# Optimization experiments

Measured on AMD Instinct MI355X. Metric: run time of the kernel, lower is better.

The kernel has to match this reference:

```python
import jax, jax.numpy as jnp
import numpy as np

NUM_EXPERTS = 8
TOP_K = 2
ENTROPY_WEIGHT = 0.1
MAX_USAGE_RATIO = 0.3


def setup_inputs() -> dict:
    key = jax.random.key(0)
    k0, k1, k2 = jax.random.split(key, 3)
    B, S, D, H, E = 4, 4096, 1024, 1024, NUM_EXPERTS
    x = jax.random.normal(k0, (B, S, D), jnp.float32)
    gate_w = jax.random.normal(k1, (D, E), jnp.float32) * (1.0 / np.sqrt(D))
    gate_b = jnp.zeros((E,), jnp.float32)
    expert_w = jax.random.normal(k2, (E, D, H), jnp.float32) * (1.0 / np.sqrt(D))
    expert_b = jnp.zeros((E, H), jnp.float32)
    return {"x": x, "gate_w": gate_w, "gate_b": gate_b,
            "expert_w": expert_w, "expert_b": expert_b}


def reference(x, gate_w, gate_b, expert_w, expert_b):
    # x: [B, S, D]; dropout omitted (eval mode / deterministic reference)
    B, S, D = x.shape
    E = gate_w.shape[1]
    H = expert_w.shape[2]
    N = B * S
    xf = x.reshape(N, D)

    gate_logits = xf @ gate_w + gate_b            # [N, E]
    gate_probs = jax.nn.softmax(gate_logits, axis=-1)
    entropy = -jnp.sum(gate_probs * jnp.log(gate_probs + 1e-10), axis=-1).mean()
    entropy_loss = ENTROPY_WEIGHT * entropy

    topk_probs, topk_idx = jax.lax.top_k(gate_probs, TOP_K)   # [N, K]
    onehot = jax.nn.one_hot(topk_idx, E, dtype=xf.dtype)       # [N, K, E]
    combine = jnp.einsum('nk,nke->ne', topk_probs, onehot)     # [N, E] gating weight per expert

    # Weighted combine of per-expert Linear outputs; loop over small fixed E.
    out = jnp.zeros((N, H), xf.dtype)
    for e in range(E):
        out = out + combine[:, e:e + 1] * (xf @ expert_w[e] + expert_b[e])

    counts = jnp.sum(onehot, axis=(0, 1))                      # [E] tokens routed per expert
    usage_ratios = counts / N
    overuse_penalty = jnp.sum(jax.nn.relu(usage_ratios - MAX_USAGE_RATIO))

    return out.reshape(B, S, H), entropy_loss + overuse_penalty
```

## Files before the change

### kernel.cpp

```cpp
#include <hip/hip_runtime.h>
#include <hip/hip_bf16.h>

typedef __bf16 bf16x8 __attribute__((ext_vector_type(8)));
typedef __bf16 bf16x4 __attribute__((ext_vector_type(4)));
typedef float  f32x4  __attribute__((ext_vector_type(4)));

#define NTOK 16384
#define DDIM 1024
#define HDIM 1024
#define NEXP 8

#define XB_OFF   0u
#define WT_OFF   33554432u
#define IDX_OFF  50331648u
#define PRB_OFF  50855936u
#define TTE_OFF  51380224u
#define TTP_OFF  51511296u
#define CNT_OFF  51642368u
#define ENT_OFF  51642400u

typedef __attribute__((address_space(1))) void gvoid_t;
typedef __attribute__((address_space(3))) void lvoid_t;

__device__ __forceinline__ void cp16(void* lds, const void* g) {
  __builtin_amdgcn_global_load_lds((gvoid_t*)g, (lvoid_t*)lds, 16, 0, 0);
}

__global__ __launch_bounds__(256) void transpose_w(const float* __restrict__ w,
                                                   __bf16* __restrict__ wT) {
  const int e  = blockIdx.z;
  const int d0 = blockIdx.y * 64;
  const int h0 = blockIdx.x * 64;
  __shared__ float tile[64][68];
  const int t = threadIdx.x;
  const float* base = w + ((size_t)e * DDIM + d0) * HDIM + h0;
#pragma unroll
  for (int it = 0; it < 4; ++it) {
    int dl = it * 16 + (t >> 4);
    int hl = (t & 15) * 4;
    float4 v = *(const float4*)(base + (size_t)dl * HDIM + hl);
    tile[dl][hl]     = v.x;
    tile[dl][hl + 1] = v.y;
    tile[dl][hl + 2] = v.z;
    tile[dl][hl + 3] = v.w;
  }
  __syncthreads();
  __bf16* obase = wT + ((size_t)e * HDIM + h0) * DDIM + d0;
#pragma unroll
  for (int it = 0; it < 4; ++it) {
    int hl = it * 16 + (t >> 4);
    int dl = (t & 15) * 4;
    bf16x4 bv;
    bv[0] = (__bf16)tile[dl][hl];
    bv[1] = (__bf16)tile[dl + 1][hl];
    bv[2] = (__bf16)tile[dl + 2][hl];
    bv[3] = (__bf16)tile[dl + 3][hl];
    *(bf16x4*)(obase + (size_t)hl * DDIM + dl) = bv;
  }
}

__global__ __launch_bounds__(256) void gate_kernel(
    const float* __restrict__ x, const float* __restrict__ gw,
    const float* __restrict__ gb, __bf16* __restrict__ xb,
    int* __restrict__ idx_g, float* __restrict__ prob_g,
    int2* __restrict__ tt_e, float2* __restrict__ tt_p,
    int* __restrict__ cnt_g, float* __restrict__ ent_g) {
  __shared__ float gwT[8 * 1040];
  __shared__ int   lidx[8 * 64];
  __shared__ float lprob[8 * 64];
  __shared__ int   lcnt[8];
  __shared__ int   gbase[8];
  __shared__ float went[4];
  const int tid = threadIdx.x, w = tid >> 6, lane = tid & 63;
  if (tid < 8) lcnt[tid] = 0;
#pragma unroll
  for (int i = 0; i < 32; ++i) {
    int lin = i * 256 + tid;
    gwT[(lin & 7) * 1040 + (lin >> 3)] = gw[lin];
  }
  __syncthreads();

  float entacc = 0.f;
  for (int t = 0; t < 8; ++t) {
    const int n = blockIdx.x * 32 + w * 8 + t;
    const float4* xr = (const float4*)(x + (size_t)n * DDIM);
    float acc[8] = {0.f, 0.f, 0.f, 0.f, 0.f, 0.f, 0.f, 0.f};
#pragma unroll
    for (int i = 0; i < 4; ++i) {
      float4 v = xr[i * 64 + lane];
      bf16x4 bv;
      bv[0] = (__bf16)v.x; bv[1] = (__bf16)v.y;
      bv[2] = (__bf16)v.z; bv[3] = (__bf16)v.w;
      *(bf16x4*)(xb + (size_t)n * DDIM + i * 256 + lane * 4) = bv;
#pragma unroll
      for (int e = 0; e < 8; ++e) {
        float4 g = *(const float4*)&gwT[e * 1040 + i * 256 + lane * 4];
        acc[e] += v.x * g.x + v.y * g.y + v.z * g.z + v.w * g.w;
      }
    }
#pragma unroll
    for (int e = 0; e < 8; ++e) {
      float s = acc[e];
      for (int off = 32; off; off >>= 1) s += __shfl_down(s, off);
      acc[e] = s;
    }
    if (lane == 0) {
      float p[8];
      float mx = -1e30f;
#pragma unroll
      for (int e = 0; e < 8; ++e) { p[e] = acc[e] + gb[e]; mx = fmaxf(mx, p[e]); }
      float s = 0.f;
#pragma unroll
      for (int e = 0; e < 8; ++e) { p[e] = expf(p[e] - mx); s += p[e]; }
      float inv = 1.0f / s;
      float ent = 0.f;
#pragma unroll
      for (int e = 0; e < 8; ++e) { p[e] *= inv; ent -= p[e] * logf(p[e] + 1e-10f); }
      entacc += ent;
      int e1 = 0; float p1 = p[0];
#pragma unroll
      for (int e = 1; e < 8; ++e) if (p[e] > p1) { p1 = p[e]; e1 = e; }
      int e2 = (e1 == 0) ? 1 : 0; float p2 = p[e2];
#pragma unroll
      for (int e = 0; e < 8; ++e) if (e != e1 && p[e] > p2) { p2 = p[e]; e2 = e; }
      tt_e[n] = make_int2(e1, e2);
      tt_p[n] = make_float2(p1, p2);
      int j = atomicAdd(&lcnt[e1], 1); lidx[e1 * 64 + j] = n; lprob[e1 * 64 + j] = p1;
      j = atomicAdd(&lcnt[e2], 1);     lidx[e2 * 64 + j] = n; lprob[e2 * 64 + j] = p2;
    }
  }
  if (lane == 0) went[w] = entacc;
  __syncthreads();
  if (tid < 8) gbase[tid] = atomicAdd(&cnt_g[tid], lcnt[tid]);
  if (tid == 0) atomicAdd(ent_g, went[0] + went[1] + went[2] + went[3]);
  __syncthreads();
#pragma unroll
  for (int e = 0; e < 8; ++e) {
    for (int j = tid; j < lcnt[e]; j += 256) {
      idx_g[e * NTOK + gbase[e] + j]  = lidx[e * 64 + j];
      prob_g[e * NTOK + gbase[e] + j] = lprob[e * 64 + j];
    }
  }
}

__global__ __launch_bounds__(256) void init_out(const int2* __restrict__ tt_e,
                                                const float2* __restrict__ tt_p,
                                                const float* __restrict__ eb,
                                                float* __restrict__ out) {
  const int n = blockIdx.x, t = threadIdx.x;
  int2   ee = tt_e[n];
  float2 pp = tt_p[n];
  float4 v1 = ((const float4*)(eb + (size_t)ee.x * HDIM))[t];
  float4 v2 = ((const float4*)(eb + (size_t)ee.y * HDIM))[t];
  float4 r;
  r.x = pp.x * v1.x + pp.y * v2.x;
  r.y = pp.x * v1.y + pp.y * v2.y;
  r.z = pp.x * v1.z + pp.y * v2.z;
  r.w = pp.x * v1.w + pp.y * v2.w;
  ((float4*)(out + (size_t)n * HDIM))[t] = r;
}

__global__ __launch_bounds__(256) void moe_gemm(
    const __bf16* __restrict__ xb, const __bf16* __restrict__ wT,
    const int* __restrict__ idx_g, const float* __restrict__ prob_g,
    const int* __restrict__ cnt_g, float* __restrict__ out) {
  const int e = blockIdx.z, gy = blockIdx.y, gx = blockIdx.x;
  const int cnt = cnt_g[e];
  if (gy * 128 >= cnt) return;

  __shared__ __bf16 Ash[128 * 64];
  __shared__ __bf16 Bsh[128 * 64];
  __shared__ int    tok_s[128];
  __shared__ float  p_s[128];

  const int tid = threadIdx.x, w = tid >> 6, lane = tid & 63;
  if (tid < 128) {
    int gm  = gy * 128 + tid;
    int src = (gm < cnt) ? gm : (cnt - 1);
    tok_s[tid] = idx_g[e * NTOK + src];
    p_s[tid]   = (gm < cnt) ? prob_g[e * NTOK + src] : 0.0f;
  }
  __syncthreads();

  f32x4 acc[4][4];
  const f32x4 zero = {0.f, 0.f, 0.f, 0.f};
#pragma unroll
  for (int mi = 0; mi < 4; ++mi)
#pragma unroll
    for (int ni = 0; ni < 4; ++ni) acc[mi][ni] = zero;

  const __bf16* wbase = wT + (size_t)e * HDIM * DDIM + (size_t)(gx * 128) * DDIM;
  const int wm = (w >> 1) * 64, wn = (w & 1) * 64;
  const int tq = lane >> 4, tr = lane & 15;
  const int rsub = lane >> 3, c = lane & 7;

  for (int kk = 0; kk < 16; ++kk) {
    const int k0 = kk * 64;
#pragma unroll
    for (int it = 0; it < 4; ++it) {
      int rb = it * 32 + w * 8;
      int r  = rb + rsub;
      cp16((char*)Ash + rb * 128,
           xb + (size_t)tok_s[r] * DDIM + k0 + c * 8);
    }
#pragma unroll
    for (int it = 0; it < 4; ++it) {
      int rb = it * 32 + w * 8;
      int r  = rb + rsub;
      cp16((char*)Bsh + rb * 128,
           wbase + (size_t)r * DDIM + k0 + c * 8);
    }
    __syncthreads();
#pragma unroll
    for (int h = 0; h < 2; ++h) {
      bf16x8 a[4], b[4];
#pragma unroll
      for (int mi = 0; mi < 4; ++mi)
        a[mi] = *(const bf16x8*)((const char*)Ash + (wm + mi * 16 + tr) * 128 + h * 64 + tq * 16);
#pragma unroll
      for (int ni = 0; ni < 4; ++ni)
        b[ni] = *(const bf16x8*)((const char*)Bsh + (wn + ni * 16 + tr) * 128 + h * 64 + tq * 16);
#pragma unroll
      for (int mi = 0; mi < 4; ++mi)
#pragma unroll
        for (int ni = 0; ni < 4; ++ni)
          acc[mi][ni] = __builtin_amdgcn_mfma_f32_16x16x32_bf16(a[mi], b[ni], acc[mi][ni], 0, 0, 0);
    }
    __syncthreads();
  }

#pragma unroll
  for (int mi = 0; mi < 4; ++mi) {
#pragma unroll
    for (int r = 0; r < 4; ++r) {
      int lr = wm + mi * 16 + tq * 4 + r;
      int gm = gy * 128 + lr;
      if (gm < cnt) {
        int   tok = tok_s[lr];
        float p   = p_s[lr];
        float* orow = out + (size_t)tok * HDIM + gx * 128 + wn + tr;
#pragma unroll
        for (int ni = 0; ni < 4; ++ni)
          atomicAdd(orow + ni * 16, p * acc[mi][ni][r]);
      }
    }
  }
}

__global__ void finalize(const float* __restrict__ ent_g, const int* __restrict__ cnt_g,
                         float* __restrict__ loss_out) {
  if (threadIdx.x == 0) {
    float ent = ent_g[0] / (float)NTOK;
    float pen = 0.f;
    for (int e = 0; e < 8; ++e) {
      float r = (float)cnt_g[e] / (float)NTOK - 0.3f;
      if (r > 0.f) pen += r;
    }
    loss_out[0] = 0.1f * ent + pen;
  }
}

extern "C" void kernel_launch(void* const* d_in, const int* in_sizes, int n_in,
                              void* d_out, int out_size, void* d_ws, size_t ws_size,
                              hipStream_t stream) {
  const float* x  = (const float*)d_in[0];
  const float* gw = (const float*)d_in[1];
  const float* gb = (const float*)d_in[2];
  const float* ew = (const float*)d_in[3];
  const float* eb = (const float*)d_in[4];
  float* out = (float*)d_out;
  char*  ws  = (char*)d_ws;

  __bf16* xb     = (__bf16*)(ws + XB_OFF);
  __bf16* wT     = (__bf16*)(ws + WT_OFF);
  int*    idx_g  = (int*)(ws + IDX_OFF);
  float*  prob_g = (float*)(ws + PRB_OFF);
  int2*   tt_e   = (int2*)(ws + TTE_OFF);
  float2* tt_p   = (float2*)(ws + TTP_OFF);
  int*    cnt_g  = (int*)(ws + CNT_OFF);
  float*  ent_g  = (float*)(ws + ENT_OFF);

  hipMemsetAsync(ws + CNT_OFF, 0, 64, stream);
  transpose_w<<<dim3(16, 16, 8), 256, 0, stream>>>(ew, wT);
  gate_kernel<<<dim3(NTOK / 32), 256, 0, stream>>>(x, gw, gb, xb, idx_g, prob_g,
                                                   tt_e, tt_p, cnt_g, ent_g);
  init_out<<<dim3(NTOK), 256, 0, stream>>>(tt_e, tt_p, eb, out);
  moe_gemm<<<dim3(8, 128, 8), 256, 0, stream>>>(xb, wT, idx_g, prob_g, cnt_g, out);
  finalize<<<1, 64, 0, stream>>>(ent_g, cnt_g, out + (size_t)NTOK * HDIM);
}
```

Measured before the change: 344.1 us.

## Group tokens by expert pair so each GEMM tile computes both experts and stores directly

Tokens are now bucketed by their (expert_lo, expert_hi) pair instead of per expert. A scan kernel builds a tile list and a scatter kernel builds the token permutation. Each GEMM block loads one A tile and two weight tiles, accumulates both experts, adds the biases and writes the output with plain stores. This removes the init_out pass and the float atomics on the output. LDS is XOR-swizzled to avoid bank conflicts, and the gate kernel keeps its weights in registers. The costs are a doubled accumulator footprint (register pressure, lower occupancy), two extra small launches, and possible tail waste because the 64 pair buckets each pad up to 128 rows.

```diff
diff --git a/kernel.cpp b/kernel.cpp
--- a/kernel.cpp
+++ b/kernel.cpp
@@ -8,16 +8,21 @@
 #define NTOK 16384
 #define DDIM 1024
 #define HDIM 1024
-#define NEXP 8
+#define CNT_STRIDE 16
 
 #define XB_OFF   0u
 #define WT_OFF   33554432u
-#define IDX_OFF  50331648u
-#define PRB_OFF  50855936u
-#define TTE_OFF  51380224u
-#define TTP_OFF  51511296u
-#define CNT_OFF  51642368u
-#define ENT_OFF  51642400u
+#define IDXP_OFF 50331648u
+#define PPP_OFF  50397184u
+#define TPID_OFF 50528256u
+#define TPP_OFF  50593792u
+#define CNT_OFF  50724864u
+#define CUR_OFF  50728960u
+#define BASE_OFF 50733056u
+#define TILT_OFF 50733312u
+#define NT_OFF   50736384u
+#define ENT_OFF  50736388u
+#define ZERO_LEN 11536u
 
 typedef __attribute__((address_space(1))) void gvoid_t;
 typedef __attribute__((address_space(3))) void lvoid_t;
@@ -28,9 +33,10 @@
 
 __global__ __launch_bounds__(256) void transpose_w(const float* __restrict__ w,
                                                    __bf16* __restrict__ wT) {
-  const int e  = blockIdx.z;
-  const int d0 = blockIdx.y * 64;
-  const int h0 = blockIdx.x * 64;
+  const int b  = blockIdx.x;
+  const int e  = b >> 8;
+  const int d0 = ((b >> 4) & 15) * 64;
+  const int h0 = (b & 15) * 64;
   __shared__ float tile[64][68];
   const int t = threadIdx.x;
   const float* base = w + ((size_t)e * DDIM + d0) * HDIM + h0;
@@ -62,202 +68,243 @@
 __global__ __launch_bounds__(256) void gate_kernel(
     const float* __restrict__ x, const float* __restrict__ gw,
     const float* __restrict__ gb, __bf16* __restrict__ xb,
-    int* __restrict__ idx_g, float* __restrict__ prob_g,
-    int2* __restrict__ tt_e, float2* __restrict__ tt_p,
+    int* __restrict__ tt_pid, float2* __restrict__ tt_pp,
     int* __restrict__ cnt_g, float* __restrict__ ent_g) {
-  __shared__ float gwT[8 * 1040];
-  __shared__ int   lidx[8 * 64];
-  __shared__ float lprob[8 * 64];
-  __shared__ int   lcnt[8];
-  __shared__ int   gbase[8];
+  __shared__ float gwT[8 * 1024];
+  __shared__ int   lcnt[64];
   __shared__ float went[4];
   const int tid = threadIdx.x, w = tid >> 6, lane = tid & 63;
-  if (tid < 8) lcnt[tid] = 0;
+  for (int i = tid; i < 64; i += 256) lcnt[i] = 0;
 #pragma unroll
   for (int i = 0; i < 32; ++i) {
     int lin = i * 256 + tid;
-    gwT[(lin & 7) * 1040 + (lin >> 3)] = gw[lin];
-  }
-  __syncthreads();
+    gwT[(lin & 7) * 1024 + (lin >> 3)] = gw[lin];
+  }
+  __syncthreads();
+  float4 gr[4][8];
+#pragma unroll
+  for (int j = 0; j < 4; ++j)
+#pragma unroll
+    for (int e = 0; e < 8; ++e)
+      gr[j][e] = *(const float4*)&gwT[e * 1024 + j * 256 + lane * 4];
+  float gbr[8];
+#pragma unroll
+  for (int e = 0; e < 8; ++e) gbr[e] = gb[e];
 
   float entacc = 0.f;
-  for (int t = 0; t < 8; ++t) {
-    const int n = blockIdx.x * 32 + w * 8 + t;
-    const float4* xr = (const float4*)(x + (size_t)n * DDIM);
+  for (int t = 0; t < 4; ++t) {
+    const int n = blockIdx.x * 16 + w * 4 + t;
     float acc[8] = {0.f, 0.f, 0.f, 0.f, 0.f, 0.f, 0.f, 0.f};
 #pragma unroll
-    for (int i = 0; i < 4; ++i) {
-      float4 v = xr[i * 64 + lane];
+    for (int j = 0; j < 4; ++j) {
+      float4 v = *(const float4*)(x + (size_t)n * DDIM + j * 256 + lane * 4);
       bf16x4 bv;
       bv[0] = (__bf16)v.x; bv[1] = (__bf16)v.y;
       bv[2] = (__bf16)v.z; bv[3] = (__bf16)v.w;
-      *(bf16x4*)(xb + (size_t)n * DDIM + i * 256 + lane * 4) = bv;
+      *(bf16x4*)(xb + (size_t)n * DDIM + j * 256 + lane * 4) = bv;
 #pragma unroll
       for (int e = 0; e < 8; ++e) {
-        float4 g = *(const float4*)&gwT[e * 1040 + i * 256 + lane * 4];
+        float4 g = gr[j][e];
         acc[e] += v.x * g.x + v.y * g.y + v.z * g.z + v.w * g.w;
       }
     }
 #pragma unroll
     for (int e = 0; e < 8; ++e) {
       float s = acc[e];
-      for (int off = 32; off; off >>= 1) s += __shfl_down(s, off);
+#pragma unroll
+      for (int off = 1; off < 64; off <<= 1) s += __shfl_xor(s, off);
       acc[e] = s;
     }
+    float p[8];
+    float mx = -1e30f;
+#pragma unroll
+    for (int e = 0; e < 8; ++e) { p[e] = acc[e] + gbr[e]; mx = fmaxf(mx, p[e]); }
+    float s = 0.f;
+#pragma unroll
+    for (int e = 0; e < 8; ++e) { p[e] = expf(p[e] - mx); s += p[e]; }
+    float inv = 1.0f / s;
+    float ent = 0.f;
+#pragma unroll
+    for (int e = 0; e < 8; ++e) { p[e] *= inv; ent -= p[e] * logf(p[e] + 1e-10f); }
+    entacc += ent;
+    int e1 = 0; float p1 = p[0];
+#pragma unroll
+    for (int e = 1; e < 8; ++e) if (p[e] > p1) { p1 = p[e]; e1 = e; }
+    int e2 = (e1 == 0) ? 1 : 0; float p2 = p[e2];
+#pragma unroll
+    for (int e = 0; e < 8; ++e) if (e != e1 && p[e] > p2) { p2 = p[e]; e2 = e; }
+    int   elo = (e1 < e2) ? e1 : e2;
+    int   ehi = (e1 < e2) ? e2 : e1;
+    float plo = (e1 < e2) ? p1 : p2;
+    float phi = (e1 < e2) ? p2 : p1;
+    int pid = elo * 8 + ehi;
     if (lane == 0) {
-      float p[8];
-      float mx = -1e30f;
-#pragma unroll
-      for (int e = 0; e < 8; ++e) { p[e] = acc[e] + gb[e]; mx = fmaxf(mx, p[e]); }
-      float s = 0.f;
-#pragma unroll
-      for (int e = 0; e < 8; ++e) { p[e] = expf(p[e] - mx); s += p[e]; }
-      float inv = 1.0f / s;
-      float ent = 0.f;
-#pragma unroll
-      for (int e = 0; e < 8; ++e) { p[e] *= inv; ent -= p[e] * logf(p[e] + 1e-10f); }
-      entacc += ent;
-      int e1 = 0; float p1 = p[0];
-#pragma unroll
-      for (int e = 1; e < 8; ++e) if (p[e] > p1) { p1 = p[e]; e1 = e; }
-      int e2 = (e1 == 0) ? 1 : 0; float p2 = p[e2];
-#pragma unroll
-      for (int e = 0; e < 8; ++e) if (e != e1 && p[e] > p2) { p2 = p[e]; e2 = e; }
-      tt_e[n] = make_int2(e1, e2);
-      tt_p[n] = make_float2(p1, p2);
-      int j = atomicAdd(&lcnt[e1], 1); lidx[e1 * 64 + j] = n; lprob[e1 * 64 + j] = p1;
-      j = atomicAdd(&lcnt[e2], 1);     lidx[e2 * 64 + j] = n; lprob[e2 * 64 + j] = p2;
+      tt_pid[n] = pid;
+      tt_pp[n]  = make_float2(plo, phi);
+      atomicAdd(&lcnt[pid], 1);
     }
   }
   if (lane == 0) went[w] = entacc;
   __syncthreads();
-  if (tid < 8) gbase[tid] = atomicAdd(&cnt_g[tid], lcnt[tid]);
-  if (tid == 0) atomicAdd(ent_g, went[0] + went[1] + went[2] + went[3]);
-  __syncthreads();
-#pragma unroll
-  for (int e = 0; e < 8; ++e) {
-    for (int j = tid; j < lcnt[e]; j += 256) {
-      idx_g[e * NTOK + gbase[e] + j]  = lidx[e * 64 + j];
-      prob_g[e * NTOK + gbase[e] + j] = lprob[e * 64 + j];
-    }
-  }
-}
-
-__global__ __launch_bounds__(256) void init_out(const int2* __restrict__ tt_e,
-                                                const float2* __restrict__ tt_p,
-                                                const float* __restrict__ eb,
-                                                float* __restrict__ out) {
-  const int n = blockIdx.x, t = threadIdx.x;
-  int2   ee = tt_e[n];
-  float2 pp = tt_p[n];
-  float4 v1 = ((const float4*)(eb + (size_t)ee.x * HDIM))[t];
-  float4 v2 = ((const float4*)(eb + (size_t)ee.y * HDIM))[t];
-  float4 r;
-  r.x = pp.x * v1.x + pp.y * v2.x;
-  r.y = pp.x * v1.y + pp.y * v2.y;
-  r.z = pp.x * v1.z + pp.y * v2.z;
-  r.w = pp.x * v1.w + pp.y * v2.w;
-  ((float4*)(out + (size_t)n * HDIM))[t] = r;
+  if (tid < 64 && lcnt[tid]) atomicAdd(&cnt_g[tid * CNT_STRIDE], lcnt[tid]);
+  if (tid == 0)
+    atomicAdd(ent_g, went[0] + went[1] + went[2] + went[3]);
+}
+
+__global__ void scan_kernel(const int* __restrict__ cnt_g, int* __restrict__ base_g,
+                            int4* __restrict__ tilt, int* __restrict__ nt_g,
+                            const float* __restrict__ ent_g, float* __restrict__ loss_out) {
+  if (threadIdx.x == 0) {
+    int b = 0, t = 0;
+    int ecnt[8] = {0, 0, 0, 0, 0, 0, 0, 0};
+    for (int pid = 0; pid < 64; ++pid) {
+      int c = cnt_g[pid * CNT_STRIDE];
+      base_g[pid] = b;
+      if (c > 0) {
+        ecnt[pid >> 3] += c;
+        ecnt[pid & 7]  += c;
+        for (int r = 0; r < c; r += 128) tilt[t++] = make_int4(pid, r, c, b);
+        b += c;
+      }
+    }
+    *nt_g = t;
+    float pen = 0.f;
+    for (int e = 0; e < 8; ++e) {
+      float r = (float)ecnt[e] / (float)NTOK - 0.3f;
+      if (r > 0.f) pen += r;
+    }
+    loss_out[0] = 0.1f * (ent_g[0] / (float)NTOK) + pen;
+  }
+}
+
+__global__ __launch_bounds__(256) void scatter_kernel(
+    const int* __restrict__ tt_pid, const float2* __restrict__ tt_pp,
+    const int* __restrict__ base_g, int* __restrict__ cur_g,
+    int* __restrict__ idx_p, float2* __restrict__ pp_p) {
+  __shared__ int lcnt[64], lbase[64];
+  const int tid = threadIdx.x;
+  if (tid < 64) lcnt[tid] = 0;
+  __syncthreads();
+  const int n = blockIdx.x * 256 + tid;
+  const int pid = tt_pid[n];
+  int lofs = atomicAdd(&lcnt[pid], 1);
+  __syncthreads();
+  if (tid < 64 && lcnt[tid]) lbase[tid] = atomicAdd(&cur_g[tid * CNT_STRIDE], lcnt[tid]);
+  __syncthreads();
+  int dst = base_g[pid] + lbase[pid] + lofs;
+  idx_p[dst] = n;
+  pp_p[dst]  = tt_pp[n];
 }
 
 __global__ __launch_bounds__(256) void moe_gemm(
     const __bf16* __restrict__ xb, const __bf16* __restrict__ wT,
-    const int* __restrict__ idx_g, const float* __restrict__ prob_g,
-    const int* __restrict__ cnt_g, float* __restrict__ out) {
-  const int e = blockIdx.z, gy = blockIdx.y, gx = blockIdx.x;
-  const int cnt = cnt_g[e];
-  if (gy * 128 >= cnt) return;
+    const float* __restrict__ eb, const int* __restrict__ idx_p,
+    const float2* __restrict__ pp_p, const int4* __restrict__ tilt,
+    const int* __restrict__ nt_g, float* __restrict__ out) {
+  const int gy = blockIdx.y;
+  if (gy >= *nt_g) return;
+  const int4 te = tilt[gy];
+  const int pid = te.x, row0 = te.y, cntp = te.z, gbase = te.w;
+  const int elo = pid >> 3, ehi = pid & 7;
+  const int gx = blockIdx.x;
 
   __shared__ __bf16 Ash[128 * 64];
-  __shared__ __bf16 Bsh[128 * 64];
+  __shared__ __bf16 BloS[128 * 64];
+  __shared__ __bf16 BhiS[128 * 64];
   __shared__ int    tok_s[128];
-  __shared__ float  p_s[128];
+  __shared__ float2 pp_s[128];
 
   const int tid = threadIdx.x, w = tid >> 6, lane = tid & 63;
   if (tid < 128) {
-    int gm  = gy * 128 + tid;
-    int src = (gm < cnt) ? gm : (cnt - 1);
-    tok_s[tid] = idx_g[e * NTOK + src];
-    p_s[tid]   = (gm < cnt) ? prob_g[e * NTOK + src] : 0.0f;
-  }
-  __syncthreads();
-
-  f32x4 acc[4][4];
+    int s = row0 + tid;
+    int g = gbase + ((s < cntp) ? s : (cntp - 1));
+    tok_s[tid] = idx_p[g];
+    pp_s[tid]  = pp_p[g];
+  }
+  __syncthreads();
+
+  f32x4 accL[4][4], accH[4][4];
   const f32x4 zero = {0.f, 0.f, 0.f, 0.f};
 #pragma unroll
   for (int mi = 0; mi < 4; ++mi)
 #pragma unroll
-    for (int ni = 0; ni < 4; ++ni) acc[mi][ni] = zero;
-
-  const __bf16* wbase = wT + (size_t)e * HDIM * DDIM + (size_t)(gx * 128) * DDIM;
+    for (int ni = 0; ni < 4; ++ni) { accL[mi][ni] = zero; accH[mi][ni] = zero; }
+
   const int wm = (w >> 1) * 64, wn = (w & 1) * 64;
-  const int tq = lane >> 4, tr = lane & 15;
-  const int rsub = lane >> 3, c = lane & 7;
+  const int tq = lane >> 4, tr = lane & 15, tr7 = tr & 7;
+  const int rsub = lane >> 3;
+  const int csw = ((lane & 7) ^ rsub) * 8;
+
+  const __bf16* wlo = wT + (size_t)elo * HDIM * DDIM + (size_t)(gx * 128) * DDIM;
+  const __bf16* whi = wT + (size_t)ehi * HDIM * DDIM + (size_t)(gx * 128) * DDIM;
+  const __bf16* aptr[4];
+  const __bf16* lptr[4];
+  const __bf16* hptr[4];
+#pragma unroll
+  for (int it = 0; it < 4; ++it) {
+    int r = it * 32 + w * 8 + rsub;
+    aptr[it] = xb + (size_t)tok_s[r] * DDIM + csw;
+    lptr[it] = wlo + (size_t)r * DDIM + csw;
+    hptr[it] = whi + (size_t)r * DDIM + csw;
+  }
 
   for (int kk = 0; kk < 16; ++kk) {
-    const int k0 = kk * 64;
 #pragma unroll
     for (int it = 0; it < 4; ++it) {
-      int rb = it * 32 + w * 8;
-      int r  = rb + rsub;
-      cp16((char*)Ash + rb * 128,
-           xb + (size_t)tok_s[r] * DDIM + k0 + c * 8);
-    }
-#pragma unroll
-    for (int it = 0; it < 4; ++it) {
-      int rb = it * 32 + w * 8;
-      int r  = rb + rsub;
-      cp16((char*)Bsh + rb * 128,
-           wbase + (size_t)r * DDIM + k0 + c * 8);
+      const int rb = it * 32 + w * 8;
+      cp16((char*)Ash  + rb * 128, aptr[it]); aptr[it] += 64;
+      cp16((char*)BloS + rb * 128, lptr[it]); lptr[it] += 64;
+      cp16((char*)BhiS + rb * 128, hptr[it]); hptr[it] += 64;
     }
     __syncthreads();
 #pragma unroll
     for (int h = 0; h < 2; ++h) {
-      bf16x8 a[4], b[4];
+      const int co = (h << 2) | tq;
+      bf16x8 a[4], bl[4], bh[4];
 #pragma unroll
       for (int mi = 0; mi < 4; ++mi)
-        a[mi] = *(const bf16x8*)((const char*)Ash + (wm + mi * 16 + tr) * 128 + h * 64 + tq * 16);
-#pragma unroll
-      for (int ni = 0; ni < 4; ++ni)
-        b[ni] = *(const bf16x8*)((const char*)Bsh + (wn + ni * 16 + tr) * 128 + h * 64 + tq * 16);
+        a[mi] = *(const bf16x8*)((const char*)Ash + (wm + mi * 16 + tr) * 128 +
+                                 ((co ^ tr7) << 4));
+#pragma unroll
+      for (int ni = 0; ni < 4; ++ni) {
+        bl[ni] = *(const bf16x8*)((const char*)BloS + (wn + ni * 16 + tr) * 128 +
+                                  ((co ^ tr7) << 4));
+        bh[ni] = *(const bf16x8*)((const char*)BhiS + (wn + ni * 16 + tr) * 128 +
+                                  ((co ^ tr7) << 4));
+      }
 #pragma unroll
       for (int mi = 0; mi < 4; ++mi)
 #pragma unroll
-        for (int ni = 0; ni < 4; ++ni)
-          acc[mi][ni] = __builtin_amdgcn_mfma_f32_16x16x32_bf16(a[mi], b[ni], acc[mi][ni], 0, 0, 0);
+        for (int ni = 0; ni < 4; ++ni) {
+          accL[mi][ni] = __builtin_amdgcn_mfma_f32_16x16x32_bf16(a[mi], bl[ni], accL[mi][ni], 0, 0, 0);
+          accH[mi][ni] = __builtin_amdgcn_mfma_f32_16x16x32_bf16(a[mi], bh[ni], accH[mi][ni], 0, 0, 0);
+        }
     }
     __syncthreads();
   }
 
-#pragma unroll
-  for (int mi = 0; mi < 4; ++mi) {
+  float blov[4], bhiv[4];
+#pragma unroll
+  for (int ni = 0; ni < 4; ++ni) {
+    int col = gx * 128 + wn + ni * 16 + tr;
+    blov[ni] = eb[elo * HDIM + col];
+    bhiv[ni] = eb[ehi * HDIM + col];
+  }
+#pragma unroll
+  for (int mi = 0; mi < 4; ++mi)
 #pragma unroll
     for (int r = 0; r < 4; ++r) {
       int lr = wm + mi * 16 + tq * 4 + r;
-      int gm = gy * 128 + lr;
-      if (gm < cnt) {
-        int   tok = tok_s[lr];
-        float p   = p_s[lr];
+      if (row0 + lr < cntp) {
+        int    tok = tok_s[lr];
+        float2 pp  = pp_s[lr];
         float* orow = out + (size_t)tok * HDIM + gx * 128 + wn + tr;
 #pragma unroll
         for (int ni = 0; ni < 4; ++ni)
-          atomicAdd(orow + ni * 16, p * acc[mi][ni][r]);
+          orow[ni * 16] = pp.x * (accL[mi][ni][r] + blov[ni]) +
+                          pp.y * (accH[mi][ni][r] + bhiv[ni]);
       }
     }
-  }
-}
-
-__global__ void finalize(const float* __restrict__ ent_g, const int* __restrict__ cnt_g,
-                         float* __restrict__ loss_out) {
-  if (threadIdx.x == 0) {
-    float ent = ent_g[0] / (float)NTOK;
-    float pen = 0.f;
-    for (int e = 0; e < 8; ++e) {
-      float r = (float)cnt_g[e] / (float)NTOK - 0.3f;
-      if (r > 0.f) pen += r;
-    }
-    loss_out[0] = 0.1f * ent + pen;
-  }
 }
 
 extern "C" void kernel_launch(void* const* d_in, const int* in_sizes, int n_in,
@@ -273,18 +320,25 @@
 
   __bf16* xb     = (__bf16*)(ws + XB_OFF);
   __bf16* wT     = (__bf16*)(ws + WT_OFF);
-  int*    idx_g  = (int*)(ws + IDX_OFF);
-  float*  prob_g = (float*)(ws + PRB_OFF);
-  int2*   tt_e   = (int2*)(ws + TTE_OFF);
-  float2* tt_p   = (float2*)(ws + TTP_OFF);
+  int*    idx_p  = (int*)(ws + IDXP_OFF);
+  float2* pp_p   = (float2*)(ws + PPP_OFF);
+  int*    tt_pid = (int*)(ws + TPID_OFF);
+  float2* tt_pp  = (float2*)(ws + TPP_OFF);
   int*    cnt_g  = (int*)(ws + CNT_OFF);
+  int*    cur_g  = (int*)(ws + CUR_OFF);
+  int*    base_g = (int*)(ws + BASE_OFF);
+  int4*   tilt   = (int4*)(ws + TILT_OFF);
+  int*    nt_g   = (int*)(ws + NT_OFF);
   float*  ent_g  = (float*)(ws + ENT_OFF);
 
-  hipMemsetAsync(ws + CNT_OFF, 0, 64, stream);
-  transpose_w<<<dim3(16, 16, 8), 256, 0, stream>>>(ew, wT);
-  gate_kernel<<<dim3(NTOK / 32), 256, 0, stream>>>(x, gw, gb, xb, idx_g, prob_g,
-                                                   tt_e, tt_p, cnt_g, ent_g);
-  init_out<<<dim3(NTOK), 256, 0, stream>>>(tt_e, tt_p, eb, out);
-  moe_gemm<<<dim3(8, 128, 8), 256, 0, stream>>>(xb, wT, idx_g, prob_g, cnt_g, out);
-  finalize<<<1, 64, 0, stream>>>(ent_g, cnt_g, out + (size_t)NTOK * HDIM);
-}
+  hipMemsetAsync(ws + CNT_OFF, 0, ZERO_LEN, stream);
+  transpose_w<<<dim3(2048), 256, 0, stream>>>(ew, wT);
+  gate_kernel<<<dim3(1024), 256, 0, stream>>>(x, gw, gb, xb, tt_pid, tt_pp,
+                                              cnt_g, ent_g);
+  scan_kernel<<<1, 64, 0, stream>>>(cnt_g, base_g, tilt, nt_g, ent_g,
+                                    out + (size_t)NTOK * HDIM);
+  scatter_kernel<<<dim3(64), 256, 0, stream>>>(tt_pid, tt_pp, base_g, cur_g,
+                                               idx_p, pp_p);
+  moe_gemm<<<dim3(8, 160), 256, 0, stream>>>(xb, wT, eb, idx_p, pp_p, tilt,
+                                             nt_g, out);
+}
```

After: 327.9 us. 1.05x faster.
